# Performance work log

Measured on AMD Instinct MI355X. Metric: run time of the kernel, lower is better.

Reference implementation:

```python
import jax, jax.numpy as jnp
import numpy as np

DIM, HEADS, HD, TOPK, SCALE = 256, 8, 32, 4, 2


def _conv1x1(x, w, b):
    # 1x1 Conv2d with folded (eval-mode) BatchNorm -> affine: weight (O,C), bias (O,)
    return jnp.einsum('bchw,oc->bohw', x, w) + b[None, :, None, None]


def setup_inputs() -> dict:
    key = jax.random.key(0)
    ks = jax.random.split(key, 12)
    b, h, w = 2, 64, 64
    hu, wu = 32, 32
    s = lambda fan: 1.0 / np.sqrt(fan)
    return {
        'x': jax.random.normal(ks[0], (b, DIM, h, w), jnp.float32),
        'upper_feat': jax.random.normal(ks[1], (b, DIM, hu, wu), jnp.float32),
        'q_w': jax.random.normal(ks[2], (DIM, DIM), jnp.float32) * s(DIM),
        'q_b': jnp.zeros((DIM,), jnp.float32),
        'kv_w': jax.random.normal(ks[3], (2 * DIM, DIM), jnp.float32) * s(DIM),
        'kv_b': jnp.zeros((2 * DIM,), jnp.float32),
        'proj_w': jax.random.normal(ks[4], (DIM, DIM), jnp.float32) * s(DIM),
        'proj_b': jnp.zeros((DIM,), jnp.float32),
        'pe_w': jax.random.normal(ks[5], (DIM, 1, 7, 7), jnp.float32) * s(49),
        'pe_b': jnp.zeros((DIM,), jnp.float32),
        'gate_w': jax.random.normal(ks[6], (HD, 2 * HD), jnp.float32) * s(2 * HD),
        'gate_b': jnp.zeros((HD,), jnp.float32),
    }


def reference(x, upper_feat, q_w, q_b, kv_w, kv_b, proj_w, proj_b, pe_w, pe_b, gate_w, gate_b):
    b, c, h, w = x.shape
    n = h * w
    _, _, hu, wu = upper_feat.shape
    nu = hu * wu
    # projections -> (b, H, seq, d)
    q = _conv1x1(x, q_w, q_b).reshape(b, HEADS, HD, n).transpose(0, 1, 3, 2)
    kv = _conv1x1(upper_feat, kv_w, kv_b).reshape(b, HEADS, 2 * HD, nu).transpose(0, 1, 3, 2)
    k, v = kv[..., :HD], kv[..., HD:]
    # coarse cross-attention (fine queries -> coarse keys)
    sim = jnp.einsum('bhnd,bhmd->bhnm', q, k) * (HD ** -0.5)  # [b,H,n,nu]
    attn = jax.nn.softmax(sim, axis=-1)
    coarse = jnp.einsum('bhnm,bhmd->bhnd', attn, v)
    # fine branch: gumbel top-k over coarse positions, gather 2x2 fine blocks
    f_kv = _conv1x1(x, kv_w, kv_b).reshape(b, HEADS, 2 * HD, n).transpose(0, 1, 3, 2)
    f_k, f_v = f_kv[..., :HD], f_kv[..., HD:]
    gsim = sim.mean(axis=2)  # [b,H,nu]
    gum = jax.random.gumbel(jax.random.key(42), gsim.shape, gsim.dtype)
    soft = jax.nn.softmax(gsim + gum, axis=-1)
    _, ti = jax.lax.top_k(soft, TOPK)  # [b,H,k]
    h_idx = (ti // wu) * SCALE
    w_idx = (ti % wu) * SCALE
    txi = jnp.concatenate([(h_idx + dh) * w + (w_idx + dw)
                           for dh in range(SCALE) for dw in range(SCALE)], axis=-1)  # [b,H,4k]
    tk = jnp.take_along_axis(f_k, txi[..., None], axis=2)  # [b,H,4k,d]
    tv = jnp.take_along_axis(f_v, txi[..., None], axis=2)
    fine = jax.nn.softmax(jnp.einsum('bhnd,bhmd->bhnm', q, tk) * (HD ** -0.5), axis=-1)
    refined = jnp.einsum('bhnm,bhmd->bhnd', fine, tv)
    # gated fusion (Conv1d kernel_size=1 == linear over channels, shared across heads)
    fus = jnp.concatenate([coarse, refined], axis=-1)  # [b,H,n,2d]
    gate = jax.nn.sigmoid(jnp.einsum('bhnc,dc->bhnd', fus, gate_w) + gate_b)
    x_out = gate * refined + (1.0 - gate) * coarse
    x_out = x_out.transpose(0, 1, 3, 2).reshape(b, c, h, w)
    # depthwise 7x7 conv PE on coarse V, upsampled bilinearly (align_corners=False)
    v_r = v.transpose(0, 1, 3, 2).reshape(b, c, hu, wu)
    v_pe = jax.lax.conv_general_dilated(
        v_r, pe_w, window_strides=(1, 1), padding=((3, 3), (3, 3)),
        dimension_numbers=('NCHW', 'OIHW', 'NCHW'), feature_group_count=c)
    v_pe = v_pe + pe_b[None, :, None, None]
    v_pe = jax.image.resize(v_pe, (b, c, h, w), method='bilinear')
    return _conv1x1(x_out + v_pe, proj_w, proj_b)
```

## Files before the change

### kernel.cpp

```cpp
#include <hip/hip_runtime.h>
#include <cstdint>
#include <cstddef>

#define SCALE_F 0.17677669529663687f
#define SHIFT_F 8.0f

typedef __bf16 bf16x8 __attribute__((ext_vector_type(8)));
typedef float  floatx4 __attribute__((ext_vector_type(4)));
#define MFMA16(a,b,c) __builtin_amdgcn_mfma_f32_16x16x32_bf16(a, b, c, 0, 0, 0)

__device__ __forceinline__ unsigned short f2bf(float x) {
  unsigned u = __float_as_uint(x);
  u += 0x7FFFu + ((u >> 16) & 1u);
  return (unsigned short)(u >> 16);
}
__device__ __forceinline__ float bf2f(unsigned short h) {
  return __uint_as_float((unsigned)h << 16);
}
union bfu { unsigned short u; __bf16 b; };
__device__ __forceinline__ __bf16 us2bf(unsigned short u) { bfu t; t.u = u; return t.b; }
__device__ __forceinline__ void bfsplit(float x, unsigned short& h, unsigned short& l) {
  h = f2bf(x);
  l = f2bf(x - bf2f(h));
}
__device__ __forceinline__ unsigned cvt_pk_bf16(float lo, float hi) {
  unsigned r;
  asm("v_cvt_pk_bf16_f32 %0, %1, %2" : "=v"(r) : "v"(lo), "v"(hi));
  return r;
}

__device__ __forceinline__ unsigned rotl32(unsigned v, int d) {
  return (v << d) | (v >> (32 - d));
}

__device__ __forceinline__ void threefry2x32(unsigned k0, unsigned k1,
                                             unsigned& x0, unsigned& x1) {
  unsigned k2 = k0 ^ k1 ^ 0x1BD11BDAu;
  x0 += k0; x1 += k1;
#define TF_R(r) { x0 += x1; x1 = rotl32(x1, r); x1 ^= x0; }
  TF_R(13) TF_R(15) TF_R(26) TF_R(6)
  x0 += k1; x1 += k2 + 1u;
  TF_R(17) TF_R(29) TF_R(16) TF_R(24)
  x0 += k2; x1 += k0 + 2u;
  TF_R(13) TF_R(15) TF_R(26) TF_R(6)
  x0 += k0; x1 += k1 + 3u;
  TF_R(17) TF_R(29) TF_R(16) TF_R(24)
  x0 += k1; x1 += k2 + 4u;
  TF_R(13) TF_R(15) TF_R(26) TF_R(6)
  x0 += k2; x1 += k0 + 5u;
#undef TF_R
}

__device__ __forceinline__ float jax_gumbel_key42(unsigned idx) {
  unsigned x0 = 0u, x1 = idx;
  threefry2x32(0u, 42u, x0, x1);
  unsigned bits = x0 ^ x1;
  unsigned fb = (bits >> 9) | 0x3f800000u;
  float f = __uint_as_float(fb) - 1.0f;
  const float tiny = 1.17549435e-38f;
  float u = f * (1.0f - tiny) + tiny;
  u = fmaxf(tiny, u);
  return -logf(-logf(u));
}

__device__ __forceinline__ float quad_xor1_add(float x) {
  int v = __builtin_amdgcn_mov_dpp(__float_as_int(x), 0xB1, 0xF, 0xF, true);
  return x + __int_as_float(v);
}
__device__ __forceinline__ float quad_xor2_add(float x) {
  int v = __builtin_amdgcn_mov_dpp(__float_as_int(x), 0x4E, 0xF, 0xF, true);
  return x + __int_as_float(v);
}

__global__ __launch_bounds__(256)
void split_w_kernel(const float* __restrict__ qw, const float* __restrict__ pw,
                    unsigned short* __restrict__ ws) {
  int i = blockIdx.x * 256 + threadIdx.x;
  unsigned short h, l;
  bfsplit(qw[i], h, l);
  ws[i] = h; ws[65536 + i] = l;
  bfsplit(pw[i], h, l);
  ws[131072 + i] = h; ws[196608 + i] = l;
}

template<int MODE>
__global__ __launch_bounds__(256)
void convmf_kernel(const unsigned short* __restrict__ WH,
                   const unsigned short* __restrict__ WL,
                   const float* __restrict__ bias,
                   const float* __restrict__ X, float* __restrict__ Y,
                   const float* __restrict__ vpe, float* __restrict__ qbar_g) {
  __shared__ __align__(16) unsigned short bhs[64 * 264];
  __shared__ __align__(16) unsigned short bls[64 * 264];
  const int tid  = threadIdx.x;
  const int lane = tid & 63;
  const int w    = tid >> 6;
  const int col  = lane & 15;
  const int quad = lane >> 4;
  const int bx = blockIdx.x, by = blockIdx.y, bz = blockIdx.z;
  const int sn0 = (tid & 15) * 4;
  const int sc0 = (tid >> 4) * 2;

  float wy0 = 0.f, wy1 = 0.f; int r0 = 0, r1 = 0;
  float wx0[4], wx1[4]; int cl0[4], cl1[4];
  if constexpr (MODE == 1) {
    float sy = 0.5f * (float)bx - 0.25f;
    int fy = (int)floorf(sy);
    wy1 = sy - (float)fy; wy0 = 1.0f - wy1;
    r0 = fy < 0 ? 0 : fy; r1 = (fy + 1) > 31 ? 31 : (fy + 1);
    #pragma unroll
    for (int k = 0; k < 4; ++k) {
      int jc = sn0 + k;
      float sx = 0.5f * (float)jc - 0.25f;
      int fx = (int)floorf(sx);
      wx1[k] = sx - (float)fx; wx0[k] = 1.0f - wx1[k];
      cl0[k] = fx < 0 ? 0 : fx; cl1[k] = (fx + 1) > 31 ? 31 : (fx + 1);
    }
  }

  const float* Xb = X + (size_t)bz * 256 * 4096 + bx * 64;

  #pragma unroll 2
  for (int s = 0; s < 8; ++s) {
    int c = s * 32 + sc0;
    float4 xa = *(const float4*)(Xb + (size_t)c * 4096 + sn0);
    float4 xb = *(const float4*)(Xb + (size_t)(c + 1) * 4096 + sn0);
    float ea[4] = {xa.x, xa.y, xa.z, xa.w};
    float eb[4] = {xb.x, xb.y, xb.z, xb.w};
    if constexpr (MODE == 1) {
      const float* vpa = vpe + ((size_t)bz * 256 + c) * 1024;
      const float* vpb = vpa + 1024;
      #pragma unroll
      for (int i = 0; i < 4; ++i) {
        ea[i] += wy0 * (wx0[i]*vpa[r0*32 + cl0[i]] + wx1[i]*vpa[r0*32 + cl1[i]])
               + wy1 * (wx0[i]*vpa[r1*32 + cl0[i]] + wx1[i]*vpa[r1*32 + cl1[i]]);
        eb[i] += wy0 * (wx0[i]*vpb[r0*32 + cl0[i]] + wx1[i]*vpb[r0*32 + cl1[i]])
               + wy1 * (wx0[i]*vpb[r1*32 + cl0[i]] + wx1[i]*vpb[r1*32 + cl1[i]]);
      }
    }
    #pragma unroll
    for (int i = 0; i < 4; ++i) {
      unsigned short ha, la, hb, lb;
      bfsplit(ea[i], ha, la);
      bfsplit(eb[i], hb, lb);
      *(unsigned*)(bhs + (sn0 + i) * 264 + c) = (unsigned)ha | ((unsigned)hb << 16);
      *(unsigned*)(bls + (sn0 + i) * 264 + c) = (unsigned)la | ((unsigned)lb << 16);
    }
  }
  __syncthreads();

  const unsigned short* wh = WH + (size_t)(by*64 + w*16 + col) * 256;
  const unsigned short* wl = WL + (size_t)(by*64 + w*16 + col) * 256;
  floatx4 f[4] = {{0.f,0.f,0.f,0.f},{0.f,0.f,0.f,0.f},{0.f,0.f,0.f,0.f},{0.f,0.f,0.f,0.f}};
  #pragma unroll
  for (int s = 0; s < 8; ++s) {
    bf16x8 ah = *(const bf16x8*)(wh + s*32 + quad*8);
    bf16x8 al = *(const bf16x8*)(wl + s*32 + quad*8);
    #pragma unroll
    for (int nt = 0; nt < 4; ++nt) {
      bf16x8 bh8 = *(const bf16x8*)(bhs + (nt*16 + col)*264 + s*32 + quad*8);
      bf16x8 bl8 = *(const bf16x8*)(bls + (nt*16 + col)*264 + s*32 + quad*8);
      f[nt] = MFMA16(ah, bh8, f[nt]);
      f[nt] = MFMA16(al, bh8, f[nt]);
      f[nt] = MFMA16(ah, bl8, f[nt]);
    }
  }

  float* Yb = Y + (size_t)bz * 256 * 4096 + bx * 64;
  #pragma unroll
  for (int r = 0; r < 4; ++r) {
    int o = by*64 + w*16 + quad*4 + r;
    float bi = bias[o];
    float rs = 0.f;
    #pragma unroll
    for (int nt = 0; nt < 4; ++nt) {
      float val = f[nt][r] + bi;
      Yb[(size_t)o*4096 + nt*16 + col] = val;
      rs += val;
    }
    if constexpr (MODE == 0) {
      rs += __shfl_xor(rs, 1); rs += __shfl_xor(rs, 2);
      rs += __shfl_xor(rs, 4); rs += __shfl_xor(rs, 8);
      if (col == 0) atomicAdd(qbar_g + bz*256 + o, rs);
    }
  }
}

__global__ __launch_bounds__(256)
void convkv_kernel(const float* __restrict__ W, const float* __restrict__ bias,
                   const float* __restrict__ X, float* __restrict__ Y,
                   float* __restrict__ Y2,
                   unsigned short* __restrict__ KH, unsigned short* __restrict__ KL,
                   unsigned short* __restrict__ VH, unsigned short* __restrict__ VL) {
  __shared__ __align__(16) float As[16][68];
  __shared__ __align__(16) float Bs[16][68];
  const int tid = threadIdx.x;
  const int tx = tid & 15, ty = tid >> 4;
  const int bx = blockIdx.x, by = blockIdx.y, bz = blockIdx.z;
  const int C = 256, N = 1024;
  const float* Xb = X + (size_t)bz * C * N + bx * 64;
  const int ar = tid >> 2;
  const int ac = (tid & 3) * 4;
  const int bc = tid >> 4;
  const int bn = (tid & 15) * 4;
  float acc[4][4] = {};

  for (int kc = 0; kc < C; kc += 16) {
    float4 av = *(const float4*)(W + (size_t)(by * 64 + ar) * C + kc + ac);
    float4 bv = *(const float4*)(Xb + (size_t)(kc + bc) * N + bn);
    As[ac+0][ar] = av.x; As[ac+1][ar] = av.y; As[ac+2][ar] = av.z; As[ac+3][ar] = av.w;
    *(float4*)&Bs[bc][bn] = bv;
    __syncthreads();
    #pragma unroll
    for (int kk = 0; kk < 16; ++kk) {
      float4 a = *(const float4*)&As[kk][ty*4];
      float4 b = *(const float4*)&Bs[kk][tx*4];
      acc[0][0] = fmaf(a.x, b.x, acc[0][0]); acc[0][1] = fmaf(a.x, b.y, acc[0][1]);
      acc[0][2] = fmaf(a.x, b.z, acc[0][2]); acc[0][3] = fmaf(a.x, b.w, acc[0][3]);
      acc[1][0] = fmaf(a.y, b.x, acc[1][0]); acc[1][1] = fmaf(a.y, b.y, acc[1][1]);
      acc[1][2] = fmaf(a.y, b.z, acc[1][2]); acc[1][3] = fmaf(a.y, b.w, acc[1][3]);
      acc[2][0] = fmaf(a.z, b.x, acc[2][0]); acc[2][1] = fmaf(a.z, b.y, acc[2][1]);
      acc[2][2] = fmaf(a.z, b.z, acc[2][2]); acc[2][3] = fmaf(a.z, b.w, acc[2][3]);
      acc[3][0] = fmaf(a.w, b.x, acc[3][0]); acc[3][1] = fmaf(a.w, b.y, acc[3][1]);
      acc[3][2] = fmaf(a.w, b.z, acc[3][2]); acc[3][3] = fmaf(a.w, b.w, acc[3][3]);
    }
    __syncthreads();
  }

  float vals[4][4];
  #pragma unroll
  for (int i = 0; i < 4; ++i) {
    float bi = bias[by*64 + ty*4 + i];
    #pragma unroll
    for (int j = 0; j < 4; ++j) vals[i][j] = acc[i][j] + bi;
  }

  #pragma unroll
  for (int i = 0; i < 4; ++i) {
    int o = by*64 + ty*4 + i;
    int hh = o >> 6, dd = o & 63;
    float* yb = Y + (size_t)bz*524288 + (size_t)hh*65536 + dd;
    #pragma unroll
    for (int j = 0; j < 4; ++j) {
      int m = bx*64 + tx*4 + j;
      yb[(size_t)m*64] = vals[i][j];
      if (dd >= 32)
        Y2[((size_t)bz*256 + hh*32 + (dd-32))*1024 + m] = vals[i][j];
    }
  }
  const int bh_ = bz*8 + by;
  const int dd0 = ty*4;
  if (dd0 < 32) {
    #pragma unroll
    for (int j = 0; j < 4; ++j) {
      int m = bx*64 + tx*4 + j;
      unsigned short h[4], l[4];
      #pragma unroll
      for (int i = 0; i < 4; ++i) bfsplit(vals[i][j], h[i], l[i]);
      uint2 ph, pl;
      ph.x = (unsigned)h[0] | ((unsigned)h[1] << 16);
      ph.y = (unsigned)h[2] | ((unsigned)h[3] << 16);
      pl.x = (unsigned)l[0] | ((unsigned)l[1] << 16);
      pl.y = (unsigned)l[2] | ((unsigned)l[3] << 16);
      *(uint2*)(KH + ((size_t)bh_*1024 + m)*32 + dd0) = ph;
      *(uint2*)(KL + ((size_t)bh_*1024 + m)*32 + dd0) = pl;
    }
  } else {
    const int m0 = bx*64 + tx*4;
    const int ml = (m0 >> 2) & 7;
    const int mp = (m0 & ~31) + ((ml & 3) << 3) + ((ml >> 2) << 2);
    #pragma unroll
    for (int i = 0; i < 4; ++i) {
      int dv = dd0 + i - 32;
      unsigned short h[4], l[4];
      #pragma unroll
      for (int j = 0; j < 4; ++j) bfsplit(vals[i][j], h[j], l[j]);
      uint2 ph, pl;
      ph.x = (unsigned)h[0] | ((unsigned)h[1] << 16);
      ph.y = (unsigned)h[2] | ((unsigned)h[3] << 16);
      pl.x = (unsigned)l[0] | ((unsigned)l[1] << 16);
      pl.y = (unsigned)l[2] | ((unsigned)l[3] << 16);
      *(uint2*)(VH + ((size_t)bh_*32 + dv)*1024 + mp) = ph;
      *(uint2*)(VL + ((size_t)bh_*32 + dv)*1024 + mp) = pl;
    }
  }
}

__global__ __launch_bounds__(256)
void stats_gather_kernel(const float* __restrict__ qbar_g, const float* __restrict__ kv_m,
                         const float* __restrict__ x, const float* __restrict__ kv_w,
                         const float* __restrict__ kv_b, float* __restrict__ fkv_g) {
  __shared__ float qbar[32];
  __shared__ float vals[1024];
  __shared__ float rv[256];
  __shared__ int ri[256];
  __shared__ int txi_s[16];
  __shared__ float xcol[16][260];
  const int tid = threadIdx.x;
  const int bh = blockIdx.x >> 2;
  const int quarter = blockIdx.x & 3;
  const int b = bh >> 3, hh = bh & 7;

  if (tid < 32) qbar[tid] = qbar_g[b*256 + hh*32 + tid] * (1.0f/4096.0f);
  __syncthreads();

  for (int m = tid; m < 1024; m += 256) {
    const float* kbp = kv_m + (size_t)bh*65536 + (size_t)m*64;
    float s = 0.f;
    #pragma unroll
    for (int d4 = 0; d4 < 8; ++d4) {
      float4 kk = *(const float4*)&kbp[d4*4];
      s = fmaf(qbar[d4*4+0], kk.x, s);
      s = fmaf(qbar[d4*4+1], kk.y, s);
      s = fmaf(qbar[d4*4+2], kk.z, s);
      s = fmaf(qbar[d4*4+3], kk.w, s);
    }
    vals[m] = s * SCALE_F + jax_gumbel_key42((unsigned)(bh*1024 + m));
  }
  __syncthreads();

  int sel[4];
  for (int t = 0; t < 4; ++t) {
    float bv = -INFINITY; int bi = 0x7fffffff;
    for (int m = tid; m < 1024; m += 256) {
      float v = vals[m];
      if (v > bv || (v == bv && m < bi)) { bv = v; bi = m; }
    }
    rv[tid] = bv; ri[tid] = bi;
    __syncthreads();
    for (int st = 128; st >= 1; st >>= 1) {
      if (tid < st) {
        float ov = rv[tid+st]; int oi = ri[tid+st];
        if (ov > rv[tid] || (ov == rv[tid] && oi < ri[tid])) { rv[tid] = ov; ri[tid] = oi; }
      }
      __syncthreads();
    }
    int w = ri[0];
    sel[t] = w;
    __syncthreads();
    if (tid == 0) vals[w] = -INFINITY;
    __syncthreads();
  }

  if (tid == 0) {
    #pragma unroll
    for (int t = 0; t < 4; ++t) {
      int ti = sel[t];
      int hi = (ti >> 5) * 2, wi = (ti & 31) * 2;
      #pragma unroll
      for (int dh = 0; dh < 2; ++dh)
        #pragma unroll
        for (int dw = 0; dw < 2; ++dw)
          txi_s[(dh*2+dw)*4 + t] = (hi+dh)*64 + (wi+dw);
    }
  }
  __syncthreads();

  #pragma unroll
  for (int i = 0; i < 16; ++i) {
    int e = tid + 256*i;
    int c = e >> 4, j = e & 15;
    xcol[j][c] = x[(size_t)b*1048576 + (size_t)c*4096 + txi_s[j]];
  }
  __syncthreads();
  const int dd = quarter*16 + (tid >> 4);
  const int j  = tid & 15;
  const int o  = hh*64 + dd;
  const float* wrow = kv_w + (size_t)o*256;
  float a0 = 0.f, a1 = 0.f, a2 = 0.f, a3 = 0.f;
  const float* xc = &xcol[j][0];
  #pragma unroll 4
  for (int c = 0; c < 256; c += 4) {
    a0 = fmaf(wrow[c+0], xc[c+0], a0);
    a1 = fmaf(wrow[c+1], xc[c+1], a1);
    a2 = fmaf(wrow[c+2], xc[c+2], a2);
    a3 = fmaf(wrow[c+3], xc[c+3], a3);
  }
  fkv_g[(size_t)bh*1024 + dd*16 + j] = ((a0+a1)+(a2+a3)) + kv_b[o];
}

__global__ __launch_bounds__(256)
void peconv_kernel(const float* __restrict__ v_ch, const float* __restrict__ pe_w,
                   const float* __restrict__ pe_b, float* __restrict__ v_pe) {
  __shared__ float vch[1024];
  __shared__ float wch[49];
  const int tid = threadIdx.x;
  const int bc = blockIdx.x;
  const int b = bc >> 8, c = bc & 255;
  const float* src = v_ch + ((size_t)b*256 + c)*1024;
  #pragma unroll
  for (int i = 0; i < 4; ++i) vch[tid + 256*i] = src[tid + 256*i];
  if (tid < 49) wch[tid] = pe_w[c*49 + tid];
  float pb = pe_b[c];
  __syncthreads();
  #pragma unroll
  for (int pi = 0; pi < 4; ++pi) {
    int p = tid + 256*pi;
    int i0 = p >> 5, j0 = p & 31;
    float s = 0.f;
    #pragma unroll
    for (int ky = 0; ky < 7; ++ky) {
      int yy = i0 + ky - 3;
      if (yy < 0 || yy > 31) continue;
      #pragma unroll
      for (int kx = 0; kx < 7; ++kx) {
        int xx = j0 + kx - 3;
        if (xx < 0 || xx > 31) continue;
        s = fmaf(wch[ky*7+kx], vch[yy*32+xx], s);
      }
    }
    v_pe[((size_t)b*256 + c)*1024 + p] = s + pb;
  }
}

__global__ __launch_bounds__(512, 2)
void attn_kernel(const float* __restrict__ q_cm,
                 const unsigned short* __restrict__ kb_h,
                 const unsigned short* __restrict__ kb_l,
                 const unsigned short* __restrict__ vb_h,
                 const unsigned short* __restrict__ vb_l,
                 const float* __restrict__ fkv_g,
                 const float* __restrict__ gate_w, const float* __restrict__ gate_b,
                 float* __restrict__ x_o) {
  __shared__ __align__(16) char smem[48256];
  float* gw_s = (float*)smem;
  float* gb_s = (float*)(smem + 9216);
  float* tk   = (float*)(smem + 9344);
  float* tv   = (float*)(smem + 11392);
  char*  region = smem + 13440;

  const int tid  = threadIdx.x;
  const int lane = tid & 63;
  const int w    = tid >> 6;
  const int qpair = w & 3;
  const int half  = w >> 2;
  const int col  = lane & 15;
  const int quad = lane >> 4;

  const int linear = blockIdx.y * 32 + blockIdx.x;
  const int xcd  = linear & 7;
  const int slot = linear >> 3;
  const int bh = xcd * 2 + (slot >> 5);
  const int nx = slot & 31;
  const int b = bh >> 3, hh = bh & 7;
  const int n0 = nx * 128;

  #pragma unroll
  for (int i = 0; i < 4; ++i) {
    int e = tid + 512*i;
    gw_s[(e >> 6)*72 + (e & 63)] = gate_w[e];
  }
  if (tid < 32) gb_s[tid] = gate_b[tid];

  if (tid < 256) {
    const float* src = fkv_g + (size_t)bh * 1024;
    #pragma unroll
    for (int i = 0; i < 4; ++i) {
      int e4 = (tid & 63) + 64 * i;
      float4 val = ((const float4*)src)[e4];
      int e = e4 * 4;
      int dd = e >> 4, j0 = e & 15;
      float* dst = (dd < 32) ? tk : tv;
      int ddv = (dd < 32) ? dd : dd - 32;
      dst[(j0+0)*32 + ddv] = val.x;
      dst[(j0+1)*32 + ddv] = val.y;
      dst[(j0+2)*32 + ddv] = val.z;
      dst[(j0+3)*32 + ddv] = val.w;
    }
  }
  __syncthreads();

  const float* qbase_cm = q_cm + ((size_t)b*256 + hh*32)*4096 + n0;
  const int qf = tid >> 2;
  const int sf = tid & 3;

  bf16x8 aqh0, aql0, aqh1, aql1;
  #pragma unroll
  for (int j = 0; j < 8; ++j) {
    float qv0 = qbase_cm[(size_t)(quad*8 + j)*4096 + qpair*32 + col];
    float qv1 = qbase_cm[(size_t)(quad*8 + j)*4096 + qpair*32 + 16 + col];
    unsigned short h, l;
    bfsplit(qv0, h, l);
    aqh0[j] = us2bf(h); aql0[j] = us2bf(l);
    bfsplit(qv1, h, l);
    aqh1[j] = us2bf(h); aql1[j] = us2bf(l);
  }

  const unsigned short* kph = kb_h + (size_t)bh * 32768;
  const unsigned short* kpl = kb_l + (size_t)bh * 32768;
  const unsigned short* vph = vb_h + (size_t)bh * 32768;
  const unsigned short* vpl = vb_l + (size_t)bh * 32768;
  const int mbase = half * 512;

#define LDKH(c, t) (*(const bf16x8*)(kph + ((size_t)(mbase + (c)*32 + (t)*16 + col))*32 + quad*8))
#define LDKL(c, t) (*(const bf16x8*)(kpl + ((size_t)(mbase + (c)*32 + (t)*16 + col))*32 + quad*8))
#define LDVH(c, t) (*(const bf16x8*)(vph + ((size_t)((t)*16 + col))*1024 + mbase + (c)*32 + quad*8))
#define LDVL(c, t) (*(const bf16x8*)(vpl + ((size_t)((t)*16 + col))*1024 + mbase + (c)*32 + quad*8))

  floatx4 oA0 = {0.f,0.f,0.f,0.f}, oA1 = {0.f,0.f,0.f,0.f};
  floatx4 oB0 = {0.f,0.f,0.f,0.f}, oB1 = {0.f,0.f,0.f,0.f};
  const floatx4 zero = {0.f, 0.f, 0.f, 0.f};
  float lsA = 0.f, lsB = 0.f;

  floatx4 sA0, sA1, sB0, sB1;
  {
    bf16x8 k0h = LDKH(0,0), k1h = LDKH(0,1);
    bf16x8 k0l = LDKL(0,0), k1l = LDKL(0,1);
    sA0 = MFMA16(k0h, aqh0, zero); sA0 = MFMA16(k0h, aql0, sA0); sA0 = MFMA16(k0l, aqh0, sA0);
    sA1 = MFMA16(k1h, aqh0, zero); sA1 = MFMA16(k1h, aql0, sA1); sA1 = MFMA16(k1l, aqh0, sA1);
    sB0 = MFMA16(k0h, aqh1, zero); sB0 = MFMA16(k0h, aql1, sB0); sB0 = MFMA16(k0l, aqh1, sB0);
    sB1 = MFMA16(k1h, aqh1, zero); sB1 = MFMA16(k1h, aql1, sB1); sB1 = MFMA16(k1l, aqh1, sB1);
  }

  for (int c = 0; c < 16; ++c) {
    bf16x8 v0h = LDVH(c,0), v1h = LDVH(c,1);
    bf16x8 v0l = LDVL(c,0), v1l = LDVL(c,1);
    bf16x8 nk0h, nk1h, nk0l, nk1l;
    if (c < 15) {
      nk0h = LDKH(c+1,0); nk1h = LDKH(c+1,1);
      nk0l = LDKL(c+1,0); nk1l = LDKL(c+1,1);
    }

    float pA0[4], pA1[4], pB0[4], pB1[4];
    #pragma unroll
    for (int r = 0; r < 4; ++r) {
      pA0[r] = __expf(fmaf(sA0[r], SCALE_F, -SHIFT_F));
      pA1[r] = __expf(fmaf(sA1[r], SCALE_F, -SHIFT_F));
      pB0[r] = __expf(fmaf(sB0[r], SCALE_F, -SHIFT_F));
      pB1[r] = __expf(fmaf(sB1[r], SCALE_F, -SHIFT_F));
      lsA += pA0[r] + pA1[r];
      lsB += pB0[r] + pB1[r];
    }
    bf16x8 paA, paB;
    ((unsigned*)&paA)[0] = cvt_pk_bf16(pA0[0], pA0[1]);
    ((unsigned*)&paA)[1] = cvt_pk_bf16(pA0[2], pA0[3]);
    ((unsigned*)&paA)[2] = cvt_pk_bf16(pA1[0], pA1[1]);
    ((unsigned*)&paA)[3] = cvt_pk_bf16(pA1[2], pA1[3]);
    ((unsigned*)&paB)[0] = cvt_pk_bf16(pB0[0], pB0[1]);
    ((unsigned*)&paB)[1] = cvt_pk_bf16(pB0[2], pB0[3]);
    ((unsigned*)&paB)[2] = cvt_pk_bf16(pB1[0], pB1[1]);
    ((unsigned*)&paB)[3] = cvt_pk_bf16(pB1[2], pB1[3]);

    if (c < 15) {
      sA0 = MFMA16(nk0h, aqh0, zero); sA0 = MFMA16(nk0h, aql0, sA0); sA0 = MFMA16(nk0l, aqh0, sA0);
      sA1 = MFMA16(nk1h, aqh0, zero); sA1 = MFMA16(nk1h, aql0, sA1); sA1 = MFMA16(nk1l, aqh0, sA1);
      sB0 = MFMA16(nk0h, aqh1, zero); sB0 = MFMA16(nk0h, aql1, sB0); sB0 = MFMA16(nk0l, aqh1, sB0);
      sB1 = MFMA16(nk1h, aqh1, zero); sB1 = MFMA16(nk1h, aql1, sB1); sB1 = MFMA16(nk1l, aqh1, sB1);
    }

    oA0 = MFMA16(paA, v0h, oA0); oA0 = MFMA16(paA, v0l, oA0);
    oA1 = MFMA16(paA, v1h, oA1); oA1 = MFMA16(paA, v1l, oA1);
    oB0 = MFMA16(paB, v0h, oB0); oB0 = MFMA16(paB, v0l, oB0);
    oB1 = MFMA16(paB, v1h, oB1); oB1 = MFMA16(paB, v1l, oB1);
  }
#undef LDKH
#undef LDKL
#undef LDVH
#undef LDVL

  lsA += __shfl_xor(lsA, 16); lsA += __shfl_xor(lsA, 32);
  lsB += __shfl_xor(lsB, 16); lsB += __shfl_xor(lsB, 32);

  {
    float* cacc = (float*)region;
    float* cl   = (float*)region + 8448;
    #pragma unroll
    for (int r = 0; r < 4; ++r) {
      int qa = qpair*32 + quad*4 + r;
      cacc[(half*128 + qa)*33 + col]      = oA0[r];
      cacc[(half*128 + qa)*33 + 16 + col] = oA1[r];
      int qb = qa + 16;
      cacc[(half*128 + qb)*33 + col]      = oB0[r];
      cacc[(half*128 + qb)*33 + 16 + col] = oB1[r];
    }
    if (quad == 0) {
      cl[half*128 + qpair*32 + col]      = lsA;
      cl[half*128 + qpair*32 + 16 + col] = lsB;
    }
  }

  float rfn[8];
  float crs[8];
  {
    float qfv[8];
    #pragma unroll
    for (int j = 0; j < 8; ++j)
      qfv[j] = qbase_cm[(size_t)(sf + 4*j)*4096 + qf];
    float p16[16]; float fl = 0.f;
    #pragma unroll
    for (int k = 0; k < 16; ++k) {
      const float* kr = tk + k*32 + sf;
      float tp = qfv[0]*kr[0];
      tp = fmaf(qfv[1], kr[4], tp);  tp = fmaf(qfv[2], kr[8], tp);
      tp = fmaf(qfv[3], kr[12], tp); tp = fmaf(qfv[4], kr[16], tp);
      tp = fmaf(qfv[5], kr[20], tp); tp = fmaf(qfv[6], kr[24], tp);
      tp = fmaf(qfv[7], kr[28], tp);
      float full = quad_xor2_add(quad_xor1_add(tp));
      float e = __expf(fmaf(full, SCALE_F, -SHIFT_F));
      p16[k] = e; fl += e;
    }
    float finv = 1.0f / fl;
    #pragma unroll
    for (int j = 0; j < 8; ++j) {
      float r = 0.f;
      #pragma unroll
      for (int k = 0; k < 16; ++k) r = fmaf(p16[k], tv[k*32 + sf + 4*j], r);
      rfn[j] = r * finv;
    }
  }
  __syncthreads();

  {
    const float* cacc = (const float*)region;
    const float* cl   = (const float*)region + 8448;
    float lt = cl[qf] + cl[128 + qf];
    float cinv = 1.0f / lt;
    #pragma unroll
    for (int j = 0; j < 8; ++j) {
      int d = sf + 4*j;
      crs[j] = (cacc[qf*33 + d] + cacc[(128 + qf)*33 + d]) * cinv;
    }
  }
  __syncthreads();

  {
    float* fus = (float*)region;
    #pragma unroll
    for (int j = 0; j < 8; ++j) {
      fus[qf*68 + sf + 4*j]      = crs[j];
      fus[qf*68 + 32 + sf + 4*j] = rfn[j];
    }
  }
  __syncthreads();

  {
    const float* fus = (const float*)region + qf*68;
    float ga[8];
    #pragma unroll
    for (int j = 0; j < 8; ++j) ga[j] = gb_s[sf + 4*j];
    #pragma unroll
    for (int c4 = 0; c4 < 16; ++c4) {
      float4 fv = *(const float4*)(fus + c4*4);
      #pragma unroll
      for (int j = 0; j < 8; ++j) {
        float4 wv = *(const float4*)(gw_s + (sf + 4*j)*72 + c4*4);
        ga[j] = fmaf(wv.x, fv.x, fmaf(wv.y, fv.y, fmaf(wv.z, fv.z, fmaf(wv.w, fv.w, ga[j]))));
      }
    }
    float* xob = x_o + ((size_t)b*256 + hh*32)*4096 + n0 + qf;
    #pragma unroll
    for (int j = 0; j < 8; ++j) {
      float g = 1.0f / (1.0f + __expf(-ga[j]));
      xob[(size_t)(sf + 4*j)*4096] = g*rfn[j] + (1.0f - g)*crs[j];
    }
  }
}

extern "C" void kernel_launch(void* const* d_in, const int* in_sizes, int n_in,
                              void* d_out, int out_size, void* d_ws, size_t ws_size,
                              hipStream_t stream) {
  const float* x      = (const float*)d_in[0];
  const float* upper  = (const float*)d_in[1];
  const float* q_w    = (const float*)d_in[2];
  const float* q_b    = (const float*)d_in[3];
  const float* kv_w   = (const float*)d_in[4];
  const float* kv_b   = (const float*)d_in[5];
  const float* proj_w = (const float*)d_in[6];
  const float* proj_b = (const float*)d_in[7];
  const float* pe_w   = (const float*)d_in[8];
  const float* pe_b   = (const float*)d_in[9];
  const float* gate_w = (const float*)d_in[10];
  const float* gate_b = (const float*)d_in[11];
  float* out = (float*)d_out;
  float* ws  = (float*)d_ws;

  float* q_cm  = ws;
  float* kv_m  = q_cm + 2097152;
  float* v_ch  = kv_m + 1048576;
  float* x_o   = v_ch + 524288;
  float* v_pe  = x_o  + 2097152;
  float* fkv_g = v_pe + 524288;
  float* qbar_g = fkv_g + 16384;
  unsigned short* kb_h = (unsigned short*)(qbar_g + 512);
  unsigned short* kb_l = kb_h + 524288;
  unsigned short* vb_h = kb_l + 524288;
  unsigned short* vb_l = vb_h + 524288;
  unsigned short* wsp  = vb_l + 524288;

  hipMemsetAsync(qbar_g, 0, 512 * sizeof(float), stream);

  split_w_kernel<<<dim3(256), 256, 0, stream>>>(q_w, proj_w, wsp);
  convmf_kernel<0><<<dim3(64, 4, 2), 256, 0, stream>>>(
      wsp, wsp + 65536, q_b, x, q_cm, nullptr, qbar_g);
  convkv_kernel<<<dim3(16, 8, 2), 256, 0, stream>>>(
      kv_w, kv_b, upper, kv_m, v_ch, kb_h, kb_l, vb_h, vb_l);
  stats_gather_kernel<<<dim3(64), 256, 0, stream>>>(
      qbar_g, kv_m, x, kv_w, kv_b, fkv_g);
  peconv_kernel<<<dim3(512), 256, 0, stream>>>(v_ch, pe_w, pe_b, v_pe);
  attn_kernel<<<dim3(32, 16), 512, 0, stream>>>(
      q_cm, kb_h, kb_l, vb_h, vb_l, fkv_g, gate_w, gate_b, x_o);
  convmf_kernel<1><<<dim3(64, 4, 2), 256, 0, stream>>>(
      wsp + 131072, wsp + 196608, proj_b, x_o, out, v_pe, nullptr);
}
```

Measured before the change: 233.2 us.

## Merge independent launches into front/mid kernels and split weights in-register

Removes the separate weight-splitting kernel. Each conv block now reads fp32 weights and splits them into bf16 hi/lo in registers before the MFMA loop. The q conv and kv conv are merged into one horizontally fused launch, and the stats/gather and PE conv kernels are merged into another. This cuts the launch count from seven to four so independent work can share the GPU. The cost is more register pressure from holding the split weights, repeated splitting of the same weights in every block, and larger shared memory per fused block, which may lower occupancy.

```diff
diff --git a/kernel.cpp b/kernel.cpp
--- a/kernel.cpp
+++ b/kernel.cpp
@@ -72,32 +72,18 @@
   return x + __int_as_float(v);
 }
 
-__global__ __launch_bounds__(256)
-void split_w_kernel(const float* __restrict__ qw, const float* __restrict__ pw,
-                    unsigned short* __restrict__ ws) {
-  int i = blockIdx.x * 256 + threadIdx.x;
-  unsigned short h, l;
-  bfsplit(qw[i], h, l);
-  ws[i] = h; ws[65536 + i] = l;
-  bfsplit(pw[i], h, l);
-  ws[131072 + i] = h; ws[196608 + i] = l;
-}
-
 template<int MODE>
-__global__ __launch_bounds__(256)
-void convmf_kernel(const unsigned short* __restrict__ WH,
-                   const unsigned short* __restrict__ WL,
-                   const float* __restrict__ bias,
-                   const float* __restrict__ X, float* __restrict__ Y,
-                   const float* __restrict__ vpe, float* __restrict__ qbar_g) {
-  __shared__ __align__(16) unsigned short bhs[64 * 264];
-  __shared__ __align__(16) unsigned short bls[64 * 264];
+__device__ __forceinline__ void convmf_body(
+    int bx, int by, int bz,
+    const float* __restrict__ W, const float* __restrict__ bias,
+    const float* __restrict__ X, float* __restrict__ Y,
+    const float* __restrict__ vpe, float* __restrict__ qbar_g,
+    unsigned short* __restrict__ bhs, unsigned short* __restrict__ bls) {
   const int tid  = threadIdx.x;
   const int lane = tid & 63;
   const int w    = tid >> 6;
   const int col  = lane & 15;
   const int quad = lane >> 4;
-  const int bx = blockIdx.x, by = blockIdx.y, bz = blockIdx.z;
   const int sn0 = (tid & 15) * 4;
   const int sc0 = (tid >> 4) * 2;
 
@@ -119,6 +105,20 @@
   }
 
   const float* Xb = X + (size_t)bz * 256 * 4096 + bx * 64;
+
+  bf16x8 wah[8], wal[8];
+  {
+    const float* wrow = W + (size_t)(by*64 + w*16 + col) * 256;
+    #pragma unroll
+    for (int s = 0; s < 8; ++s) {
+      #pragma unroll
+      for (int j = 0; j < 8; ++j) {
+        unsigned short h, l;
+        bfsplit(wrow[s*32 + quad*8 + j], h, l);
+        wah[s][j] = us2bf(h); wal[s][j] = us2bf(l);
+      }
+    }
+  }
 
   #pragma unroll 2
   for (int s = 0; s < 8; ++s) {
@@ -149,20 +149,16 @@
   }
   __syncthreads();
 
-  const unsigned short* wh = WH + (size_t)(by*64 + w*16 + col) * 256;
-  const unsigned short* wl = WL + (size_t)(by*64 + w*16 + col) * 256;
   floatx4 f[4] = {{0.f,0.f,0.f,0.f},{0.f,0.f,0.f,0.f},{0.f,0.f,0.f,0.f},{0.f,0.f,0.f,0.f}};
   #pragma unroll
   for (int s = 0; s < 8; ++s) {
-    bf16x8 ah = *(const bf16x8*)(wh + s*32 + quad*8);
-    bf16x8 al = *(const bf16x8*)(wl + s*32 + quad*8);
     #pragma unroll
     for (int nt = 0; nt < 4; ++nt) {
       bf16x8 bh8 = *(const bf16x8*)(bhs + (nt*16 + col)*264 + s*32 + quad*8);
       bf16x8 bl8 = *(const bf16x8*)(bls + (nt*16 + col)*264 + s*32 + quad*8);
-      f[nt] = MFMA16(ah, bh8, f[nt]);
-      f[nt] = MFMA16(al, bh8, f[nt]);
-      f[nt] = MFMA16(ah, bl8, f[nt]);
+      f[nt] = MFMA16(wah[s], bh8, f[nt]);
+      f[nt] = MFMA16(wal[s], bh8, f[nt]);
+      f[nt] = MFMA16(wah[s], bl8, f[nt]);
     }
   }
 
@@ -186,17 +182,16 @@
   }
 }
 
-__global__ __launch_bounds__(256)
-void convkv_kernel(const float* __restrict__ W, const float* __restrict__ bias,
-                   const float* __restrict__ X, float* __restrict__ Y,
-                   float* __restrict__ Y2,
-                   unsigned short* __restrict__ KH, unsigned short* __restrict__ KL,
-                   unsigned short* __restrict__ VH, unsigned short* __restrict__ VL) {
-  __shared__ __align__(16) float As[16][68];
-  __shared__ __align__(16) float Bs[16][68];
+__device__ __forceinline__ void convkv_body(
+    int bx, int by, int bz,
+    const float* __restrict__ W, const float* __restrict__ bias,
+    const float* __restrict__ X, float* __restrict__ Y,
+    float* __restrict__ Y2,
+    unsigned short* __restrict__ KH, unsigned short* __restrict__ KL,
+    unsigned short* __restrict__ VH, unsigned short* __restrict__ VL,
+    float (*As)[68], float (*Bs)[68]) {
   const int tid = threadIdx.x;
   const int tx = tid & 15, ty = tid >> 4;
-  const int bx = blockIdx.x, by = blockIdx.y, bz = blockIdx.z;
   const int C = 256, N = 1024;
   const float* Xb = X + (size_t)bz * C * N + bx * 64;
   const int ar = tid >> 2;
@@ -287,130 +282,164 @@
 }
 
 __global__ __launch_bounds__(256)
-void stats_gather_kernel(const float* __restrict__ qbar_g, const float* __restrict__ kv_m,
-                         const float* __restrict__ x, const float* __restrict__ kv_w,
-                         const float* __restrict__ kv_b, float* __restrict__ fkv_g) {
+void front_kernel(const float* __restrict__ q_w, const float* __restrict__ q_b,
+                  const float* __restrict__ x, float* __restrict__ q_cm,
+                  float* __restrict__ qbar_g,
+                  const float* __restrict__ kv_w, const float* __restrict__ kv_b,
+                  const float* __restrict__ upper,
+                  float* __restrict__ kv_m, float* __restrict__ v_ch,
+                  unsigned short* __restrict__ KH, unsigned short* __restrict__ KL,
+                  unsigned short* __restrict__ VH, unsigned short* __restrict__ VL) {
+  __shared__ __align__(16) unsigned short bhs[64 * 264];
+  __shared__ __align__(16) unsigned short bls[64 * 264];
+  __shared__ __align__(16) float As[16][68];
+  __shared__ __align__(16) float Bs[16][68];
+  if (blockIdx.x < 256) {
+    int idx = blockIdx.x;
+    convkv_body(idx & 15, (idx >> 4) & 7, idx >> 7,
+                kv_w, kv_b, upper, kv_m, v_ch, KH, KL, VH, VL, As, Bs);
+  } else {
+    int idx = blockIdx.x - 256;
+    convmf_body<0>(idx & 63, (idx >> 6) & 3, idx >> 8,
+                   q_w, q_b, x, q_cm, nullptr, qbar_g, bhs, bls);
+  }
+}
+
+__global__ __launch_bounds__(256)
+void mid_kernel(const float* __restrict__ qbar_g, const float* __restrict__ kv_m,
+                const float* __restrict__ x, const float* __restrict__ kv_w,
+                const float* __restrict__ kv_b, float* __restrict__ fkv_g,
+                const float* __restrict__ v_ch, const float* __restrict__ pe_w,
+                const float* __restrict__ pe_b, float* __restrict__ v_pe) {
   __shared__ float qbar[32];
   __shared__ float vals[1024];
   __shared__ float rv[256];
   __shared__ int ri[256];
   __shared__ int txi_s[16];
   __shared__ float xcol[16][260];
-  const int tid = threadIdx.x;
-  const int bh = blockIdx.x >> 2;
-  const int quarter = blockIdx.x & 3;
-  const int b = bh >> 3, hh = bh & 7;
-
-  if (tid < 32) qbar[tid] = qbar_g[b*256 + hh*32 + tid] * (1.0f/4096.0f);
-  __syncthreads();
-
-  for (int m = tid; m < 1024; m += 256) {
-    const float* kbp = kv_m + (size_t)bh*65536 + (size_t)m*64;
-    float s = 0.f;
-    #pragma unroll
-    for (int d4 = 0; d4 < 8; ++d4) {
-      float4 kk = *(const float4*)&kbp[d4*4];
-      s = fmaf(qbar[d4*4+0], kk.x, s);
-      s = fmaf(qbar[d4*4+1], kk.y, s);
-      s = fmaf(qbar[d4*4+2], kk.z, s);
-      s = fmaf(qbar[d4*4+3], kk.w, s);
-    }
-    vals[m] = s * SCALE_F + jax_gumbel_key42((unsigned)(bh*1024 + m));
-  }
-  __syncthreads();
-
-  int sel[4];
-  for (int t = 0; t < 4; ++t) {
-    float bv = -INFINITY; int bi = 0x7fffffff;
-    for (int m = tid; m < 1024; m += 256) {
-      float v = vals[m];
-      if (v > bv || (v == bv && m < bi)) { bv = v; bi = m; }
-    }
-    rv[tid] = bv; ri[tid] = bi;
-    __syncthreads();
-    for (int st = 128; st >= 1; st >>= 1) {
-      if (tid < st) {
-        float ov = rv[tid+st]; int oi = ri[tid+st];
-        if (ov > rv[tid] || (ov == rv[tid] && oi < ri[tid])) { rv[tid] = ov; ri[tid] = oi; }
-      }
-      __syncthreads();
-    }
-    int w = ri[0];
-    sel[t] = w;
-    __syncthreads();
-    if (tid == 0) vals[w] = -INFINITY;
-    __syncthreads();
-  }
-
-  if (tid == 0) {
-    #pragma unroll
-    for (int t = 0; t < 4; ++t) {
-      int ti = sel[t];
-      int hi = (ti >> 5) * 2, wi = (ti & 31) * 2;
-      #pragma unroll
-      for (int dh = 0; dh < 2; ++dh)
-        #pragma unroll
-        for (int dw = 0; dw < 2; ++dw)
-          txi_s[(dh*2+dw)*4 + t] = (hi+dh)*64 + (wi+dw);
-    }
-  }
-  __syncthreads();
-
-  #pragma unroll
-  for (int i = 0; i < 16; ++i) {
-    int e = tid + 256*i;
-    int c = e >> 4, j = e & 15;
-    xcol[j][c] = x[(size_t)b*1048576 + (size_t)c*4096 + txi_s[j]];
-  }
-  __syncthreads();
-  const int dd = quarter*16 + (tid >> 4);
-  const int j  = tid & 15;
-  const int o  = hh*64 + dd;
-  const float* wrow = kv_w + (size_t)o*256;
-  float a0 = 0.f, a1 = 0.f, a2 = 0.f, a3 = 0.f;
-  const float* xc = &xcol[j][0];
-  #pragma unroll 4
-  for (int c = 0; c < 256; c += 4) {
-    a0 = fmaf(wrow[c+0], xc[c+0], a0);
-    a1 = fmaf(wrow[c+1], xc[c+1], a1);
-    a2 = fmaf(wrow[c+2], xc[c+2], a2);
-    a3 = fmaf(wrow[c+3], xc[c+3], a3);
-  }
-  fkv_g[(size_t)bh*1024 + dd*16 + j] = ((a0+a1)+(a2+a3)) + kv_b[o];
-}
-
-__global__ __launch_bounds__(256)
-void peconv_kernel(const float* __restrict__ v_ch, const float* __restrict__ pe_w,
-                   const float* __restrict__ pe_b, float* __restrict__ v_pe) {
   __shared__ float vch[1024];
   __shared__ float wch[49];
   const int tid = threadIdx.x;
-  const int bc = blockIdx.x;
-  const int b = bc >> 8, c = bc & 255;
-  const float* src = v_ch + ((size_t)b*256 + c)*1024;
-  #pragma unroll
-  for (int i = 0; i < 4; ++i) vch[tid + 256*i] = src[tid + 256*i];
-  if (tid < 49) wch[tid] = pe_w[c*49 + tid];
-  float pb = pe_b[c];
-  __syncthreads();
-  #pragma unroll
-  for (int pi = 0; pi < 4; ++pi) {
-    int p = tid + 256*pi;
-    int i0 = p >> 5, j0 = p & 31;
-    float s = 0.f;
-    #pragma unroll
-    for (int ky = 0; ky < 7; ++ky) {
-      int yy = i0 + ky - 3;
-      if (yy < 0 || yy > 31) continue;
-      #pragma unroll
-      for (int kx = 0; kx < 7; ++kx) {
-        int xx = j0 + kx - 3;
-        if (xx < 0 || xx > 31) continue;
-        s = fmaf(wch[ky*7+kx], vch[yy*32+xx], s);
+
+  if (blockIdx.x < 64) {
+    const int bh = blockIdx.x >> 2;
+    const int quarter = blockIdx.x & 3;
+    const int b = bh >> 3, hh = bh & 7;
+
+    if (tid < 32) qbar[tid] = qbar_g[b*256 + hh*32 + tid] * (1.0f/4096.0f);
+    __syncthreads();
+
+    for (int m = tid; m < 1024; m += 256) {
+      const float* kbp = kv_m + (size_t)bh*65536 + (size_t)m*64;
+      float s = 0.f;
+      #pragma unroll
+      for (int d4 = 0; d4 < 8; ++d4) {
+        float4 kk = *(const float4*)&kbp[d4*4];
+        s = fmaf(qbar[d4*4+0], kk.x, s);
+        s = fmaf(qbar[d4*4+1], kk.y, s);
+        s = fmaf(qbar[d4*4+2], kk.z, s);
+        s = fmaf(qbar[d4*4+3], kk.w, s);
       }
-    }
-    v_pe[((size_t)b*256 + c)*1024 + p] = s + pb;
-  }
+      vals[m] = s * SCALE_F + jax_gumbel_key42((unsigned)(bh*1024 + m));
+    }
+    __syncthreads();
+
+    int sel[4];
+    for (int t = 0; t < 4; ++t) {
+      float bv = -INFINITY; int bi = 0x7fffffff;
+      for (int m = tid; m < 1024; m += 256) {
+        float v = vals[m];
+        if (v > bv || (v == bv && m < bi)) { bv = v; bi = m; }
+      }
+      rv[tid] = bv; ri[tid] = bi;
+      __syncthreads();
+      for (int st = 128; st >= 1; st >>= 1) {
+        if (tid < st) {
+          float ov = rv[tid+st]; int oi = ri[tid+st];
+          if (ov > rv[tid] || (ov == rv[tid] && oi < ri[tid])) { rv[tid] = ov; ri[tid] = oi; }
+        }
+        __syncthreads();
+      }
+      int w = ri[0];
+      sel[t] = w;
+      __syncthreads();
+      if (tid == 0) vals[w] = -INFINITY;
+      __syncthreads();
+    }
+
+    if (tid == 0) {
+      #pragma unroll
+      for (int t = 0; t < 4; ++t) {
+        int ti = sel[t];
+        int hi = (ti >> 5) * 2, wi = (ti & 31) * 2;
+        #pragma unroll
+        for (int dh = 0; dh < 2; ++dh)
+          #pragma unroll
+          for (int dw = 0; dw < 2; ++dw)
+            txi_s[(dh*2+dw)*4 + t] = (hi+dh)*64 + (wi+dw);
+      }
+    }
+    __syncthreads();
+
+    #pragma unroll
+    for (int i = 0; i < 16; ++i) {
+      int e = tid + 256*i;
+      int c = e >> 4, j = e & 15;
+      xcol[j][c] = x[(size_t)b*1048576 + (size_t)c*4096 + txi_s[j]];
+    }
+    __syncthreads();
+    const int dd = quarter*16 + (tid >> 4);
+    const int j  = tid & 15;
+    const int o  = hh*64 + dd;
+    const float* wrow = kv_w + (size_t)o*256;
+    float a0 = 0.f, a1 = 0.f, a2 = 0.f, a3 = 0.f;
+    const float* xc = &xcol[j][0];
+    #pragma unroll 4
+    for (int c = 0; c < 256; c += 4) {
+      a0 = fmaf(wrow[c+0], xc[c+0], a0);
+      a1 = fmaf(wrow[c+1], xc[c+1], a1);
+      a2 = fmaf(wrow[c+2], xc[c+2], a2);
+      a3 = fmaf(wrow[c+3], xc[c+3], a3);
+    }
+    fkv_g[(size_t)bh*1024 + dd*16 + j] = ((a0+a1)+(a2+a3)) + kv_b[o];
+  } else {
+    const int bc = blockIdx.x - 64;
+    const int b = bc >> 8, c = bc & 255;
+    const float* src = v_ch + ((size_t)b*256 + c)*1024;
+    #pragma unroll
+    for (int i = 0; i < 4; ++i) vch[tid + 256*i] = src[tid + 256*i];
+    if (tid < 49) wch[tid] = pe_w[c*49 + tid];
+    float pb = pe_b[c];
+    __syncthreads();
+    #pragma unroll
+    for (int pi = 0; pi < 4; ++pi) {
+      int p = tid + 256*pi;
+      int i0 = p >> 5, j0 = p & 31;
+      float s = 0.f;
+      #pragma unroll
+      for (int ky = 0; ky < 7; ++ky) {
+        int yy = i0 + ky - 3;
+        if (yy < 0 || yy > 31) continue;
+        #pragma unroll
+        for (int kx = 0; kx < 7; ++kx) {
+          int xx = j0 + kx - 3;
+          if (xx < 0 || xx > 31) continue;
+          s = fmaf(wch[ky*7+kx], vch[yy*32+xx], s);
+        }
+      }
+      v_pe[((size_t)b*256 + c)*1024 + p] = s + pb;
+    }
+  }
+}
+
+__global__ __launch_bounds__(256)
+void proj_kernel(const float* __restrict__ proj_w, const float* __restrict__ proj_b,
+                 const float* __restrict__ x_o, float* __restrict__ out,
+                 const float* __restrict__ vpe) {
+  __shared__ __align__(16) unsigned short bhs[64 * 264];
+  __shared__ __align__(16) unsigned short bls[64 * 264];
+  convmf_body<1>(blockIdx.x, blockIdx.y, blockIdx.z,
+                 proj_w, proj_b, x_o, out, vpe, nullptr, bhs, bls);
 }
 
 __global__ __launch_bounds__(512, 2)
@@ -685,20 +714,16 @@
   unsigned short* kb_l = kb_h + 524288;
   unsigned short* vb_h = kb_l + 524288;
   unsigned short* vb_l = vb_h + 524288;
-  unsigned short* wsp  = vb_l + 524288;
 
   hipMemsetAsync(qbar_g, 0, 512 * sizeof(float), stream);
 
-  split_w_kernel<<<dim3(256), 256, 0, stream>>>(q_w, proj_w, wsp);
-  convmf_kernel<0><<<dim3(64, 4, 2), 256, 0, stream>>>(
-      wsp, wsp + 65536, q_b, x, q_cm, nullptr, qbar_g);
-  convkv_kernel<<<dim3(16, 8, 2), 256, 0, stream>>>(
+  front_kernel<<<dim3(768), 256, 0, stream>>>(
+      q_w, q_b, x, q_cm, qbar_g,
       kv_w, kv_b, upper, kv_m, v_ch, kb_h, kb_l, vb_h, vb_l);
-  stats_gather_kernel<<<dim3(64), 256, 0, stream>>>(
-      qbar_g, kv_m, x, kv_w, kv_b, fkv_g);
-  peconv_kernel<<<dim3(512), 256, 0, stream>>>(v_ch, pe_w, pe_b, v_pe);
+  mid_kernel<<<dim3(576), 256, 0, stream>>>(
+      qbar_g, kv_m, x, kv_w, kv_b, fkv_g, v_ch, pe_w, pe_b, v_pe);
   attn_kernel<<<dim3(32, 16), 512, 0, stream>>>(
       q_cm, kb_h, kb_l, vb_h, vb_l, fkv_g, gate_w, gate_b, x_o);
-  convmf_kernel<1><<<dim3(64, 4, 2), 256, 0, stream>>>(
-      wsp + 131072, wsp + 196608, proj_b, x_o, out, v_pe, nullptr);
-}
+  proj_kernel<<<dim3(64, 4, 2), 256, 0, stream>>>(
+      proj_w, proj_b, x_o, out, v_pe);
+}
```

Measured after the change: 216.2 us. -7.3%, faster.
